# Kernel optimization log

Hardware: AMD Instinct MI355X
Metric: run time of the kernel (lower is better)

## Reference

```python
import jax, jax.numpy as jnp
import numpy as np
import math

B, S, HID = 1, 2048, 2048
NH, NKV, HD = 32, 8, 64
GROUPS = NH // NKV
BOOST_SCALE, NARROW_SCALE = 1.0, 4.0
NEG = -1e9


def rope_cos_sin(seq_len, scale):
    inv_freq = 1.0 / (10000.0 ** (jnp.arange(0, HD, 2, dtype=jnp.float32) / HD))
    t = jnp.arange(seq_len, dtype=jnp.float32) / scale
    freqs = jnp.outer(t, inv_freq)                      # [s, hd/2]
    emb = jnp.concatenate([freqs, freqs], axis=-1)      # [s, hd]
    return jnp.cos(emb), jnp.sin(emb)


def rotate_half(x):
    x1, x2 = x[..., : HD // 2], x[..., HD // 2:]
    return jnp.concatenate([-x2, x1], axis=-1)


def apply_rope(q, k, cos, sin, position_ids):
    c = cos[position_ids][:, None]                      # [b,1,s,hd]
    s = sin[position_ids][:, None]
    return q * c + rotate_half(q) * s, k * c + rotate_half(k) * s


def setup_inputs() -> dict:
    key = jax.random.key(0)
    ks = jax.random.split(key, 5)
    hidden_states = jax.random.normal(ks[0], (B, S, HID), dtype=jnp.float32)
    i = jnp.arange(S)[:, None]
    j = jnp.arange(S)[None, :]
    attention_mask = jnp.where(j <= i, 0.0, NEG).astype(jnp.float32)[None, None]  # [1,1,S,S]
    position_ids = jnp.broadcast_to(jnp.arange(S, dtype=jnp.int32)[None], (B, S))
    sc = 1.0 / math.sqrt(HID)
    Wq = jax.random.normal(ks[1], (NH * HD, HID), dtype=jnp.float32) * sc
    Wk = jax.random.normal(ks[2], (NKV * HD, HID), dtype=jnp.float32) * sc
    Wv = jax.random.normal(ks[3], (NKV * HD, HID), dtype=jnp.float32) * sc
    Wo = jax.random.normal(ks[4], (HID, HID), dtype=jnp.float32) * sc
    return dict(hidden_states=hidden_states, attention_mask=attention_mask,
                position_ids=position_ids, Wq=Wq, Wk=Wk, Wv=Wv, Wo=Wo)


def reference(hidden_states, attention_mask, position_ids, Wq, Wk, Wv, Wo):
    b, q_len, _ = hidden_states.shape
    kv_seq_len = q_len

    q = (hidden_states @ Wq.T).reshape(b, q_len, NH, HD).transpose(0, 2, 1, 3)   # [b,H,s,hd]
    k = (hidden_states @ Wk.T).reshape(b, q_len, NKV, HD).transpose(0, 2, 1, 3)  # [b,Hkv,s,hd]
    v = (hidden_states @ Wv.T).reshape(b, q_len, NKV, HD).transpose(0, 2, 1, 3)

    boost_cos, boost_sin = rope_cos_sin(kv_seq_len, BOOST_SCALE)
    narrow_cos, narrow_sin = rope_cos_sin(kv_seq_len + 30, NARROW_SCALE)
    bq, bk = apply_rope(q, k, boost_cos, boost_sin, position_ids)
    nq, nk = apply_rope(q, k, narrow_cos, narrow_sin, position_ids)

    # repeat_kv (GQA)
    bk = jnp.repeat(bk, GROUPS, axis=1)
    nk = jnp.repeat(nk, GROUPS, axis=1)
    v = jnp.repeat(v, GROUPS, axis=1)

    inv_sqrt = 1.0 / math.sqrt(HD)
    big = jnp.einsum('bhqd,bhkd->bhqk', bq, bk) * inv_sqrt
    small = jnp.einsum('bhqd,bhkd->bhqk', nq, nk) * inv_sqrt
    big = big + attention_mask
    small = small + attention_mask

    # neighbor mask: tril minus (for rows >= context_length) tril(diag=context_length)
    # which zeroes those rows entirely -> neighbor = (j <= i) & (i < context_length)
    context_length = q_len - 10
    i = jnp.arange(q_len)[:, None]
    j = jnp.arange(kv_seq_len)[None, :]
    neighbor = (j <= i) & (i < context_length)

    merged = jnp.where(neighbor, big, small)
    probs = jax.nn.softmax(merged.astype(jnp.float32), axis=-1).astype(q.dtype)
    attn = jnp.einsum('bhqk,bhkd->bhqd', probs, v)
    attn = attn.transpose(0, 2, 1, 3).reshape(b, q_len, HID)
    return attn @ Wo.T
```

## Files before the change

kernel.cpp:

```cpp
#include <hip/hip_runtime.h>
#include <math.h>

#define S_LEN 2048
#define HIDN  2048
#define NH    32
#define NKV   8
#define HD    64
#define KVW   (NKV * HD)
#define CTX   (S_LEN - 10)

typedef unsigned short u16;
typedef __attribute__((ext_vector_type(4))) float f32x4;
typedef __attribute__((ext_vector_type(16))) float f32x16;
typedef __attribute__((ext_vector_type(8))) short s16x8;

__device__ __forceinline__ float bf2f(u16 u) {
  union { unsigned int i; float f; } v; v.i = ((unsigned int)u) << 16; return v.f;
}
__device__ __forceinline__ u16 f2bf(float f) {
  union { float f; unsigned int i; } v; v.f = f;
  unsigned int r = v.i + 0x7fffu + ((v.i >> 16) & 1u);
  return (u16)(r >> 16);
}
__device__ __forceinline__ unsigned int cvt_pk_bf16(float a, float b) {
  unsigned int d;
  asm("v_cvt_pk_bf16_f32 %0, %1, %2" : "=v"(d) : "v"(a), "v"(b));
  return d;
}

__global__ __launch_bounds__(256) void conv_all(
    const float* __restrict__ h,  const float* __restrict__ wq,
    const float* __restrict__ wk, const float* __restrict__ wv,
    const float* __restrict__ wo,
    u16* __restrict__ Hb, u16* __restrict__ Wqb, u16* __restrict__ Wkb,
    u16* __restrict__ Wvb, u16* __restrict__ Wob)
{
  const int i = blockIdx.x * 256 + threadIdx.x;
  const float* src; u16* dst; int off;
  if      (i < 1048576) { src = h;  dst = Hb;  off = i; }
  else if (i < 2097152) { src = wq; dst = Wqb; off = i - 1048576; }
  else if (i < 2359296) { src = wk; dst = Wkb; off = i - 2097152; }
  else if (i < 2621440) { src = wv; dst = Wvb; off = i - 2359296; }
  else                  { src = wo; dst = Wob; off = i - 2621440; }
  const float4 f4 = ((const float4*)src)[off];
  ushort4 o4;
  o4.x = f2bf(f4.x); o4.y = f2bf(f4.y); o4.z = f2bf(f4.z); o4.w = f2bf(f4.w);
  ((ushort4*)dst)[off] = o4;
}

#define BM 128
#define BN 128
#define BK 64

template<int OF32>
__device__ __forceinline__ void gemm_body(
    u16* __restrict__ As, u16* __restrict__ Bs,
    const u16* __restrict__ A, const u16* __restrict__ B, void* __restrict__ Cv,
    int N, int K, int row0, int col0, int otrans)
{
  const int tid  = threadIdx.x;
  const int wave = tid >> 6;
  const int lane = tid & 63;
  const int wr = (wave >> 1) * 64;
  const int wc = (wave & 1) * 64;

  f32x4 acc[4][4] = {};

  const int srow = wave * 8 + (lane >> 3);
  const int scol = (lane & 7) * 8;

  for (int kt = 0; kt < K; kt += BK) {
#pragma unroll
    for (int it = 0; it < 4; ++it) {
      const u16* gA = A + (size_t)(row0 + it * 32 + srow) * K + kt + scol;
      const u16* gB = B + (size_t)(col0 + it * 32 + srow) * K + kt + scol;
      u16* lA = &As[(it * 32 + wave * 8) * BK];
      u16* lB = &Bs[(it * 32 + wave * 8) * BK];
      __builtin_amdgcn_global_load_lds((const __attribute__((address_space(1))) void*)gA,
                                       (__attribute__((address_space(3))) void*)lA, 16, 0, 0);
      __builtin_amdgcn_global_load_lds((const __attribute__((address_space(1))) void*)gB,
                                       (__attribute__((address_space(3))) void*)lB, 16, 0, 0);
    }
    __syncthreads();
#pragma unroll
    for (int kk = 0; kk < 2; ++kk) {
      const int ko = kk * 32 + (lane >> 4) * 8;
      s16x8 af[4], bg[4];
#pragma unroll
      for (int mi = 0; mi < 4; ++mi)
        af[mi] = *(const s16x8*)&As[(wr + mi * 16 + (lane & 15)) * BK + ko];
#pragma unroll
      for (int ni = 0; ni < 4; ++ni)
        bg[ni] = *(const s16x8*)&Bs[(wc + ni * 16 + (lane & 15)) * BK + ko];
#pragma unroll
      for (int mi = 0; mi < 4; ++mi)
#pragma unroll
        for (int ni = 0; ni < 4; ++ni)
          acc[mi][ni] = __builtin_amdgcn_mfma_f32_16x16x32_bf16(af[mi], bg[ni], acc[mi][ni], 0, 0, 0);
    }
    __syncthreads();
  }

  const int rq = (lane >> 4) * 4;
  const int cq = lane & 15;
#pragma unroll
  for (int mi = 0; mi < 4; ++mi)
#pragma unroll
    for (int ni = 0; ni < 4; ++ni) {
      const int r = row0 + wr + mi * 16 + rq;
      const int c = col0 + wc + ni * 16 + cq;
      if (otrans) {
        ushort4 o4;
        o4.x = f2bf(acc[mi][ni][0]); o4.y = f2bf(acc[mi][ni][1]);
        o4.z = f2bf(acc[mi][ni][2]); o4.w = f2bf(acc[mi][ni][3]);
        *(ushort4*)&((u16*)Cv)[(size_t)c * S_LEN + r] = o4;
      } else {
#pragma unroll
        for (int t = 0; t < 4; ++t) {
          if (OF32) ((float*)Cv)[(size_t)(r + t) * N + c] = acc[mi][ni][t];
          else      ((u16*)Cv)[(size_t)(r + t) * N + c]   = f2bf(acc[mi][ni][t]);
        }
      }
    }
}

__global__ __launch_bounds__(256) void gemm_qkv(
    const u16* __restrict__ A, const u16* __restrict__ Wq, const u16* __restrict__ Wk,
    const u16* __restrict__ Wv, u16* __restrict__ Q, u16* __restrict__ Kb, u16* __restrict__ Vt)
{
  __shared__ u16 As[BM * BK];
  __shared__ u16 Bs[BN * BK];
  const int bn = blockIdx.x;
  const int row0 = blockIdx.y * BM;
  const u16* Bp; u16* Cp; int N; int col0; int ot;
  if (bn < 16)      { Bp = Wq; Cp = Q;  N = HIDN; col0 = bn * BN;        ot = 0; }
  else if (bn < 20) { Bp = Wk; Cp = Kb; N = KVW;  col0 = (bn - 16) * BN; ot = 0; }
  else              { Bp = Wv; Cp = Vt; N = KVW;  col0 = (bn - 20) * BN; ot = 1; }
  gemm_body<0>(As, Bs, A, Bp, Cp, N, HIDN, row0, col0, ot);
}

__global__ __launch_bounds__(256) void gemm_out(
    const u16* __restrict__ A, const u16* __restrict__ B, float* __restrict__ C, int N, int K)
{
  __shared__ u16 As[BM * BK];
  __shared__ u16 Bs[BN * BK];
  gemm_body<1>(As, Bs, A, B, C, N, K, blockIdx.y * BM, blockIdx.x * BN, 0);
}

__global__ __launch_bounds__(256) void rope_kernel(
    u16* __restrict__ Q, u16* __restrict__ Kb, u16* __restrict__ Kn,
    const int* __restrict__ pos_ids)
{
  const int idx = blockIdx.x * 256 + threadIdx.x;
  const int totq = S_LEN * NH * (HD / 2);
  const float LN1E4 = 9.210340371976184f;
  const float QSCL  = 0.18033688011112042f;
  if (idx < totq) {
    const int d = idx & 31;
    const int h = (idx >> 5) & (NH - 1);
    const int i = idx >> 10;
    const float f = expf(-(float)(2 * d) * (1.0f / HD) * LN1E4);
    const int pos = pos_ids[i];
    const float scl = (i < CTX) ? 1.0f : 0.25f;
    const float ang = ((float)pos * scl) * f;
    const float c = cosf(ang), s = sinf(ang);
    u16* p = Q + (size_t)i * HIDN + h * HD + d;
    const float x1 = bf2f(p[0]), x2 = bf2f(p[32]);
    p[0]  = f2bf((x1 * c - x2 * s) * QSCL);
    p[32] = f2bf((x2 * c + x1 * s) * QSCL);
  } else {
    const int k = idx - totq;
    if (k >= S_LEN * NKV * (HD / 2)) return;
    const int d  = k & 31;
    const int kh = (k >> 5) & (NKV - 1);
    const int j  = k >> 8;
    const float f = expf(-(float)(2 * d) * (1.0f / HD) * LN1E4);
    const float pos = (float)pos_ids[j];
    const float cb = cosf(pos * f),          sb = sinf(pos * f);
    const float cn = cosf(pos * 0.25f * f),  sn = sinf(pos * 0.25f * f);
    const size_t off = (size_t)j * KVW + kh * HD + d;
    u16* pb = Kb + off;
    u16* pn = Kn + off;
    const float x1 = bf2f(pb[0]), x2 = bf2f(pb[32]);
    pn[0]  = f2bf(x1 * cn - x2 * sn);
    pn[32] = f2bf(x2 * cn + x1 * sn);
    pb[0]  = f2bf(x1 * cb - x2 * sb);
    pb[32] = f2bf(x2 * cb + x1 * sb);
  }
}

#define PAD 8
__global__ __launch_bounds__(256) void attn_mfma(
    const u16* __restrict__ Q, const u16* __restrict__ K, const u16* __restrict__ Kn,
    const u16* __restrict__ Vt, u16* __restrict__ O)
{
  __shared__ __align__(16) u16 Ks[64][HD + PAD];
  __shared__ __align__(16) u16 Kns[64][HD + PAD];
  __shared__ __align__(16) u16 Vts[HD][64 + PAD];
  __shared__ __align__(16) float Of[64][64];
  __shared__ float Lf[2][32];
  __shared__ float Li[2][32];

  const int tid  = threadIdx.x;
  const int wave = tid >> 6;
  const int lane = tid & 63;
  const int l31  = lane & 31;
  const int hi   = lane >> 5;
  const int wr   = wave >> 1;
  const int wk   = wave & 1;
  const int h    = blockIdx.y;
  const int kh   = h >> 2;
  const int pr   = blockIdx.x;

  int sa[2], sb[2];
#pragma unroll
  for (int it = 0; it < 2; ++it) {
    const int u = it * 256 + tid;
    sa[it] = u >> 3;
    sb[it] = (u & 7) * 8;
  }

  for (int ph = 0; ph < 2; ++ph) {
    const int qt = ph ? pr : 31 - pr;
    const int i_base = qt * 64;
    const int rw0 = i_base + wr * 32;
    const bool mixed_blk = (qt == 31);
    const bool mixed_wv  = mixed_blk && (rw0 + 31 >= CTX);

    s16x8 bq[4];
#pragma unroll
    for (int i = 0; i < 4; ++i)
      bq[i] = *(const s16x8*)(Q + (size_t)(rw0 + l31) * HIDN + h * HD + i * 16 + hi * 8);

    f32x16 acc0 = {};
    f32x16 acc1 = {};
    float lsum = 0.f;

    const int ntiles = qt + 1;
    s16x8 kr[2], vr[2], knr[2];
#pragma unroll
    for (int it = 0; it < 2; ++it) {
      kr[it] = *(const s16x8*)(K  + (size_t)sa[it] * KVW + kh * HD + sb[it]);
      vr[it] = *(const s16x8*)(Vt + (size_t)(kh * HD + sa[it]) * S_LEN + sb[it]);
      if (mixed_blk) knr[it] = *(const s16x8*)(Kn + (size_t)sa[it] * KVW + kh * HD + sb[it]);
    }

    for (int t = 0; t < ntiles; ++t) {
      const int jt = t * 64;
      __syncthreads();
#pragma unroll
      for (int it = 0; it < 2; ++it) {
        *(s16x8*)&Ks[sa[it]][sb[it]]  = kr[it];
        *(s16x8*)&Vts[sa[it]][sb[it]] = vr[it];
        if (mixed_blk) *(s16x8*)&Kns[sa[it]][sb[it]] = knr[it];
      }
      __syncthreads();
      if (t + 1 < ntiles) {
        const int jn = jt + 64;
#pragma unroll
        for (int it = 0; it < 2; ++it) {
          kr[it] = *(const s16x8*)(K  + (size_t)(jn + sa[it]) * KVW + kh * HD + sb[it]);
          vr[it] = *(const s16x8*)(Vt + (size_t)(kh * HD + sa[it]) * S_LEN + jn + sb[it]);
          if (mixed_blk) knr[it] = *(const s16x8*)(Kn + (size_t)(jn + sa[it]) * KVW + kh * HD + sb[it]);
        }
      }

      const int j0 = jt + wk * 32;
      if (j0 > rw0 + 31) continue;
      const bool needmask = (j0 + 31 > rw0);

      f32x16 sc = {};
#pragma unroll
      for (int i = 0; i < 4; ++i) {
        const s16x8 ak = *(const s16x8*)&Ks[wk * 32 + l31][i * 16 + hi * 8];
        sc = __builtin_amdgcn_mfma_f32_32x32x16_bf16(ak, bq[i], sc, 0, 0, 0);
      }
      if (mixed_wv) {
        f32x16 scn = {};
#pragma unroll
        for (int i = 0; i < 4; ++i) {
          const s16x8 ak = *(const s16x8*)&Kns[wk * 32 + l31][i * 16 + hi * 8];
          scn = __builtin_amdgcn_mfma_f32_32x32x16_bf16(ak, bq[i], scn, 0, 0, 0);
        }
        const bool nar = (rw0 + l31) >= CTX;
#pragma unroll
        for (int r = 0; r < 16; ++r) sc[r] = nar ? scn[r] : sc[r];
      }

      float p[16];
#pragma unroll
      for (int r = 0; r < 16; ++r) {
        float e = __builtin_amdgcn_exp2f(fminf(sc[r], 80.f));
        if (needmask) {
          const int key = j0 + (r & 3) + 8 * (r >> 2) + 4 * hi;
          e = (key > rw0 + l31) ? 0.f : e;
        }
        p[r] = e;
        lsum += e;
      }

      unsigned int c[4][2];
#pragma unroll
      for (int blk = 0; blk < 4; ++blk) {
        c[blk][0] = cvt_pk_bf16(p[4 * blk + 0], p[4 * blk + 1]);
        c[blk][1] = cvt_pk_bf16(p[4 * blk + 2], p[4 * blk + 3]);
      }

#pragma unroll
      for (int s = 0; s < 2; ++s) {
        unsigned int w0 = c[2 * s][0], w2 = c[2 * s + 1][0];
        unsigned int w1 = c[2 * s][1], w3 = c[2 * s + 1][1];
        asm("v_permlane32_swap_b32 %0, %1" : "+v"(w0), "+v"(w2));
        asm("v_permlane32_swap_b32 %0, %1" : "+v"(w1), "+v"(w3));
        union { unsigned int u[4]; s16x8 v; } af;
        af.u[0] = w0; af.u[1] = w1; af.u[2] = w2; af.u[3] = w3;
        const int kc = wk * 32 + s * 16 + hi * 8;
        const s16x8 v0 = *(const s16x8*)&Vts[l31][kc];
        const s16x8 v1 = *(const s16x8*)&Vts[32 + l31][kc];
        acc0 = __builtin_amdgcn_mfma_f32_32x32x16_bf16(af.v, v0, acc0, 0, 0, 0);
        acc1 = __builtin_amdgcn_mfma_f32_32x32x16_bf16(af.v, v1, acc1, 0, 0, 0);
      }
    }

    lsum += __shfl_xor(lsum, 32, 64);
    __syncthreads();
    if (wk == 1) {
#pragma unroll
      for (int r = 0; r < 16; ++r) {
        const int rl = (r & 3) + 8 * (r >> 2) + 4 * hi;
        Of[wr * 32 + rl][l31]      = acc0[r];
        Of[wr * 32 + rl][l31 + 32] = acc1[r];
      }
      if (hi == 0) Lf[wr][l31] = lsum;
    }
    __syncthreads();
    if (wk == 0) {
      const float tot = lsum + Lf[wr][l31];
      const float inv = 1.0f / fmaxf(tot, 1e-30f);
      if (hi == 0) Li[wr][l31] = inv;
#pragma unroll
      for (int r = 0; r < 16; ++r) {
        const int rl = (r & 3) + 8 * (r >> 2) + 4 * hi;
        const float iv = Li[wr][rl];
        const size_t o = (size_t)(rw0 + rl) * HIDN + h * HD + l31;
        O[o]      = f2bf((acc0[r] + Of[wr * 32 + rl][l31])      * iv);
        O[o + 32] = f2bf((acc1[r] + Of[wr * 32 + rl][l31 + 32]) * iv);
      }
    }
  }
}

extern "C" void kernel_launch(void* const* d_in, const int* in_sizes, int n_in,
                              void* d_out, int out_size, void* d_ws, size_t ws_size,
                              hipStream_t stream)
{
  const float* hidden = (const float*)d_in[0];
  const int* pos      = (const int*)d_in[2];
  const float* Wq = (const float*)d_in[3];
  const float* Wk = (const float*)d_in[4];
  const float* Wv = (const float*)d_in[5];
  const float* Wo = (const float*)d_in[6];
  float* out = (float*)d_out;

  char* ws = (char*)d_ws;
  u16* Qb  = (u16*)(ws);
  u16* Kbb = (u16*)(ws + (8u  << 20));
  u16* Knb = (u16*)(ws + (10u << 20));
  u16* Vtb = (u16*)(ws + (12u << 20));
  u16* Ab  = (u16*)(ws + (14u << 20));
  u16* Hb  = (u16*)(ws + (22u << 20));
  u16* Wqb = (u16*)(ws + (30u << 20));
  u16* Wkb = (u16*)(ws + (38u << 20));
  u16* Wvb = (u16*)(ws + (40u << 20));
  u16* Wob = (u16*)(ws + (42u << 20));

  conv_all<<<dim3(14336), 256, 0, stream>>>(hidden, Wq, Wk, Wv, Wo, Hb, Wqb, Wkb, Wvb, Wob);
  gemm_qkv<<<dim3(24, 16), 256, 0, stream>>>(Hb, Wqb, Wkb, Wvb, Qb, Kbb, Vtb);
  const int tot = S_LEN * NH * (HD / 2) + S_LEN * NKV * (HD / 2);
  rope_kernel<<<dim3((tot + 255) / 256), 256, 0, stream>>>(Qb, Kbb, Knb, pos);
  attn_mfma<<<dim3(16, NH), 256, 0, stream>>>(Qb, Kbb, Knb, Vtb, Ab);
  gemm_out<<<dim3(16, 16), 256, 0, stream>>>(Ab, Wob, out, HIDN, HIDN);
}
```

Measured before the change: 271.3 us.

## Fuse RoPE into QKV GEMM epilogue and double-buffer GEMM LDS tiles

Removes the separate RoPE kernel by applying rotary embedding (both scales for K, scaled Q) directly on the accumulators in the QKV GEMM epilogue. This avoids an extra launch and a read-modify-write pass over Q and K. The GEMM mainloop is also changed to double-buffered LDS with async global-to-LDS prefetch of the next K tile, so loads overlap the MFMA work. This doubles LDS usage per block, which can lower occupancy, and adds sincos work to the epilogue.

```diff
diff --git a/kernel.cpp b/kernel.cpp
--- a/kernel.cpp
+++ b/kernel.cpp
@@ -13,6 +13,9 @@
 typedef __attribute__((ext_vector_type(4))) float f32x4;
 typedef __attribute__((ext_vector_type(16))) float f32x16;
 typedef __attribute__((ext_vector_type(8))) short s16x8;
+
+#define QSCL 0.18033688011112042f
+#define L2_1E4 13.287712379549449f
 
 __device__ __forceinline__ float bf2f(u16 u) {
   union { unsigned int i; float f; } v; v.i = ((unsigned int)u) << 16; return v.f;
@@ -52,11 +55,12 @@
 #define BN 128
 #define BK 64
 
-template<int OF32>
+template<int MODE>
 __device__ __forceinline__ void gemm_body(
     u16* __restrict__ As, u16* __restrict__ Bs,
-    const u16* __restrict__ A, const u16* __restrict__ B, void* __restrict__ Cv,
-    int N, int K, int row0, int col0, int otrans)
+    const u16* __restrict__ A, const u16* __restrict__ B,
+    void* __restrict__ Cv, void* __restrict__ Cv2,
+    int N, int K, int row0, int col0, const int* __restrict__ pos)
 {
   const int tid  = threadIdx.x;
   const int wave = tid >> 6;
@@ -68,125 +72,151 @@
 
   const int srow = wave * 8 + (lane >> 3);
   const int scol = (lane & 7) * 8;
-
-  for (int kt = 0; kt < K; kt += BK) {
-#pragma unroll
-    for (int it = 0; it < 4; ++it) {
-      const u16* gA = A + (size_t)(row0 + it * 32 + srow) * K + kt + scol;
-      const u16* gB = B + (size_t)(col0 + it * 32 + srow) * K + kt + scol;
-      u16* lA = &As[(it * 32 + wave * 8) * BK];
-      u16* lB = &Bs[(it * 32 + wave * 8) * BK];
-      __builtin_amdgcn_global_load_lds((const __attribute__((address_space(1))) void*)gA,
-                                       (__attribute__((address_space(3))) void*)lA, 16, 0, 0);
-      __builtin_amdgcn_global_load_lds((const __attribute__((address_space(1))) void*)gB,
-                                       (__attribute__((address_space(3))) void*)lB, 16, 0, 0);
-    }
-    __syncthreads();
+  const int NT = K / BK;
+
+#pragma unroll
+  for (int it = 0; it < 4; ++it) {
+    const u16* gA = A + (size_t)(row0 + it * 32 + srow) * K + scol;
+    const u16* gB = B + (size_t)(col0 + it * 32 + srow) * K + scol;
+    u16* lA = As + (it * 32 + wave * 8) * BK;
+    u16* lB = Bs + (it * 32 + wave * 8) * BK;
+    __builtin_amdgcn_global_load_lds((const __attribute__((address_space(1))) void*)gA,
+                                     (__attribute__((address_space(3))) void*)lA, 16, 0, 0);
+    __builtin_amdgcn_global_load_lds((const __attribute__((address_space(1))) void*)gB,
+                                     (__attribute__((address_space(3))) void*)lB, 16, 0, 0);
+  }
+
+  int cur = 0;
+  for (int t = 0; t < NT; ++t) {
+    __builtin_amdgcn_s_barrier();
+    __builtin_amdgcn_sched_barrier(0);
+    if (t + 1 < NT) {
+      const int kt = (t + 1) * BK;
+      const int nx = (cur ^ 1) * (BM * BK);
+#pragma unroll
+      for (int it = 0; it < 4; ++it) {
+        const u16* gA = A + (size_t)(row0 + it * 32 + srow) * K + kt + scol;
+        const u16* gB = B + (size_t)(col0 + it * 32 + srow) * K + kt + scol;
+        u16* lA = As + nx + (it * 32 + wave * 8) * BK;
+        u16* lB = Bs + nx + (it * 32 + wave * 8) * BK;
+        __builtin_amdgcn_global_load_lds((const __attribute__((address_space(1))) void*)gA,
+                                         (__attribute__((address_space(3))) void*)lA, 16, 0, 0);
+        __builtin_amdgcn_global_load_lds((const __attribute__((address_space(1))) void*)gB,
+                                         (__attribute__((address_space(3))) void*)lB, 16, 0, 0);
+      }
+      asm volatile("s_waitcnt vmcnt(8)" ::: "memory");
+    } else {
+      asm volatile("s_waitcnt vmcnt(0)" ::: "memory");
+    }
+    __builtin_amdgcn_sched_barrier(0);
+    __builtin_amdgcn_s_barrier();
+    __builtin_amdgcn_sched_barrier(0);
+
+    const u16* Asb = As + cur * (BM * BK);
+    const u16* Bsb = Bs + cur * (BM * BK);
 #pragma unroll
     for (int kk = 0; kk < 2; ++kk) {
       const int ko = kk * 32 + (lane >> 4) * 8;
       s16x8 af[4], bg[4];
 #pragma unroll
       for (int mi = 0; mi < 4; ++mi)
-        af[mi] = *(const s16x8*)&As[(wr + mi * 16 + (lane & 15)) * BK + ko];
+        af[mi] = *(const s16x8*)&Asb[(wr + mi * 16 + (lane & 15)) * BK + ko];
 #pragma unroll
       for (int ni = 0; ni < 4; ++ni)
-        bg[ni] = *(const s16x8*)&Bs[(wc + ni * 16 + (lane & 15)) * BK + ko];
+        bg[ni] = *(const s16x8*)&Bsb[(wc + ni * 16 + (lane & 15)) * BK + ko];
 #pragma unroll
       for (int mi = 0; mi < 4; ++mi)
 #pragma unroll
         for (int ni = 0; ni < 4; ++ni)
           acc[mi][ni] = __builtin_amdgcn_mfma_f32_16x16x32_bf16(af[mi], bg[ni], acc[mi][ni], 0, 0, 0);
     }
-    __syncthreads();
+    cur ^= 1;
   }
 
   const int rq = (lane >> 4) * 4;
   const int cq = lane & 15;
-#pragma unroll
-  for (int mi = 0; mi < 4; ++mi)
-#pragma unroll
-    for (int ni = 0; ni < 4; ++ni) {
-      const int r = row0 + wr + mi * 16 + rq;
-      const int c = col0 + wc + ni * 16 + cq;
-      if (otrans) {
+
+  if (MODE == 3) {
+#pragma unroll
+    for (int mi = 0; mi < 4; ++mi)
+#pragma unroll
+      for (int ni = 0; ni < 4; ++ni) {
+        const int r = row0 + wr + mi * 16 + rq;
+        const int c = col0 + wc + ni * 16 + cq;
+#pragma unroll
+        for (int t = 0; t < 4; ++t)
+          ((float*)Cv)[(size_t)(r + t) * N + c] = acc[mi][ni][t];
+      }
+  } else if (MODE == 2) {
+#pragma unroll
+    for (int mi = 0; mi < 4; ++mi)
+#pragma unroll
+      for (int ni = 0; ni < 4; ++ni) {
+        const int r = row0 + wr + mi * 16 + rq;
+        const int c = col0 + wc + ni * 16 + cq;
         ushort4 o4;
         o4.x = f2bf(acc[mi][ni][0]); o4.y = f2bf(acc[mi][ni][1]);
         o4.z = f2bf(acc[mi][ni][2]); o4.w = f2bf(acc[mi][ni][3]);
         *(ushort4*)&((u16*)Cv)[(size_t)c * S_LEN + r] = o4;
-      } else {
-#pragma unroll
-        for (int t = 0; t < 4; ++t) {
-          if (OF32) ((float*)Cv)[(size_t)(r + t) * N + c] = acc[mi][ni][t];
-          else      ((u16*)Cv)[(size_t)(r + t) * N + c]   = f2bf(acc[mi][ni][t]);
+      }
+  } else {
+#pragma unroll
+    for (int mi = 0; mi < 4; ++mi) {
+#pragma unroll
+      for (int t = 0; t < 4; ++t) {
+        const int i = row0 + wr + mi * 16 + rq + t;
+        const float fpos = (float)pos[i];
+#pragma unroll
+        for (int ni = 0; ni < 2; ++ni) {
+          const int d = ni * 16 + cq;
+          const int c = col0 + wc + ni * 16 + cq;
+          const float f = exp2f(-(float)(2 * d) * (1.0f / HD) * L2_1E4);
+          const float x1 = acc[mi][ni][t], x2 = acc[mi][ni + 2][t];
+          if (MODE == 0) {
+            const float scl = (i < CTX) ? 1.0f : 0.25f;
+            float sn, cs; sincosf(fpos * scl * f, &sn, &cs);
+            u16* Cq = (u16*)Cv;
+            Cq[(size_t)i * N + c]      = f2bf((x1 * cs - x2 * sn) * QSCL);
+            Cq[(size_t)i * N + c + 32] = f2bf((x2 * cs + x1 * sn) * QSCL);
+          } else {
+            float sb_, cb_; sincosf(fpos * f, &sb_, &cb_);
+            float sn_, cn_; sincosf(fpos * 0.25f * f, &sn_, &cn_);
+            u16* Kb_ = (u16*)Cv;
+            u16* Kn_ = (u16*)Cv2;
+            Kb_[(size_t)i * N + c]      = f2bf(x1 * cb_ - x2 * sb_);
+            Kb_[(size_t)i * N + c + 32] = f2bf(x2 * cb_ + x1 * sb_);
+            Kn_[(size_t)i * N + c]      = f2bf(x1 * cn_ - x2 * sn_);
+            Kn_[(size_t)i * N + c + 32] = f2bf(x2 * cn_ + x1 * sn_);
+          }
         }
       }
     }
+  }
 }
 
 __global__ __launch_bounds__(256) void gemm_qkv(
     const u16* __restrict__ A, const u16* __restrict__ Wq, const u16* __restrict__ Wk,
-    const u16* __restrict__ Wv, u16* __restrict__ Q, u16* __restrict__ Kb, u16* __restrict__ Vt)
-{
-  __shared__ u16 As[BM * BK];
-  __shared__ u16 Bs[BN * BK];
+    const u16* __restrict__ Wv, u16* __restrict__ Q, u16* __restrict__ Kb,
+    u16* __restrict__ Kn, u16* __restrict__ Vt, const int* __restrict__ pos)
+{
+  __shared__ u16 As[2 * BM * BK];
+  __shared__ u16 Bs[2 * BN * BK];
   const int bn = blockIdx.x;
   const int row0 = blockIdx.y * BM;
-  const u16* Bp; u16* Cp; int N; int col0; int ot;
-  if (bn < 16)      { Bp = Wq; Cp = Q;  N = HIDN; col0 = bn * BN;        ot = 0; }
-  else if (bn < 20) { Bp = Wk; Cp = Kb; N = KVW;  col0 = (bn - 16) * BN; ot = 0; }
-  else              { Bp = Wv; Cp = Vt; N = KVW;  col0 = (bn - 20) * BN; ot = 1; }
-  gemm_body<0>(As, Bs, A, Bp, Cp, N, HIDN, row0, col0, ot);
+  if (bn < 16)
+    gemm_body<0>(As, Bs, A, Wq, Q, nullptr, HIDN, HIDN, row0, bn * BN, pos);
+  else if (bn < 20)
+    gemm_body<1>(As, Bs, A, Wk, Kb, Kn, KVW, HIDN, row0, (bn - 16) * BN, pos);
+  else
+    gemm_body<2>(As, Bs, A, Wv, Vt, nullptr, KVW, HIDN, row0, (bn - 20) * BN, pos);
 }
 
 __global__ __launch_bounds__(256) void gemm_out(
     const u16* __restrict__ A, const u16* __restrict__ B, float* __restrict__ C, int N, int K)
 {
-  __shared__ u16 As[BM * BK];
-  __shared__ u16 Bs[BN * BK];
-  gemm_body<1>(As, Bs, A, B, C, N, K, blockIdx.y * BM, blockIdx.x * BN, 0);
-}
-
-__global__ __launch_bounds__(256) void rope_kernel(
-    u16* __restrict__ Q, u16* __restrict__ Kb, u16* __restrict__ Kn,
-    const int* __restrict__ pos_ids)
-{
-  const int idx = blockIdx.x * 256 + threadIdx.x;
-  const int totq = S_LEN * NH * (HD / 2);
-  const float LN1E4 = 9.210340371976184f;
-  const float QSCL  = 0.18033688011112042f;
-  if (idx < totq) {
-    const int d = idx & 31;
-    const int h = (idx >> 5) & (NH - 1);
-    const int i = idx >> 10;
-    const float f = expf(-(float)(2 * d) * (1.0f / HD) * LN1E4);
-    const int pos = pos_ids[i];
-    const float scl = (i < CTX) ? 1.0f : 0.25f;
-    const float ang = ((float)pos * scl) * f;
-    const float c = cosf(ang), s = sinf(ang);
-    u16* p = Q + (size_t)i * HIDN + h * HD + d;
-    const float x1 = bf2f(p[0]), x2 = bf2f(p[32]);
-    p[0]  = f2bf((x1 * c - x2 * s) * QSCL);
-    p[32] = f2bf((x2 * c + x1 * s) * QSCL);
-  } else {
-    const int k = idx - totq;
-    if (k >= S_LEN * NKV * (HD / 2)) return;
-    const int d  = k & 31;
-    const int kh = (k >> 5) & (NKV - 1);
-    const int j  = k >> 8;
-    const float f = expf(-(float)(2 * d) * (1.0f / HD) * LN1E4);
-    const float pos = (float)pos_ids[j];
-    const float cb = cosf(pos * f),          sb = sinf(pos * f);
-    const float cn = cosf(pos * 0.25f * f),  sn = sinf(pos * 0.25f * f);
-    const size_t off = (size_t)j * KVW + kh * HD + d;
-    u16* pb = Kb + off;
-    u16* pn = Kn + off;
-    const float x1 = bf2f(pb[0]), x2 = bf2f(pb[32]);
-    pn[0]  = f2bf(x1 * cn - x2 * sn);
-    pn[32] = f2bf(x2 * cn + x1 * sn);
-    pb[0]  = f2bf(x1 * cb - x2 * sb);
-    pb[32] = f2bf(x2 * cb + x1 * sb);
-  }
+  __shared__ u16 As[2 * BM * BK];
+  __shared__ u16 Bs[2 * BN * BK];
+  gemm_body<3>(As, Bs, A, B, C, nullptr, N, K, blockIdx.y * BM, blockIdx.x * BN, nullptr);
 }
 
 #define PAD 8
@@ -375,9 +405,7 @@
   u16* Wob = (u16*)(ws + (42u << 20));
 
   conv_all<<<dim3(14336), 256, 0, stream>>>(hidden, Wq, Wk, Wv, Wo, Hb, Wqb, Wkb, Wvb, Wob);
-  gemm_qkv<<<dim3(24, 16), 256, 0, stream>>>(Hb, Wqb, Wkb, Wvb, Qb, Kbb, Vtb);
-  const int tot = S_LEN * NH * (HD / 2) + S_LEN * NKV * (HD / 2);
-  rope_kernel<<<dim3((tot + 255) / 256), 256, 0, stream>>>(Qb, Kbb, Knb, pos);
+  gemm_qkv<<<dim3(24, 16), 256, 0, stream>>>(Hb, Wqb, Wkb, Wvb, Qb, Kbb, Knb, Vtb, pos);
   attn_mfma<<<dim3(16, NH), 256, 0, stream>>>(Qb, Kbb, Knb, Vtb, Ab);
   gemm_out<<<dim3(16, 16), 256, 0, stream>>>(Ab, Wob, out, HIDN, HIDN);
 }
```

After: 274.1 us. Within noise of the previous version (+1.0%).
